# Kernel optimization log

Hardware: AMD Instinct MI355X
Metric: run time of the kernel (lower is better)

Reference implementation:

```python
import jax, jax.numpy as jnp
import numpy as np

NUM_HEADS = 16
HEAD_SIZE = 64
N_EMBD = 1024
BLOCK_SIZE = 2048
B, T = 4, 2048


def setup_inputs() -> dict:
    key = jax.random.key(0)
    ks = jax.random.split(key, 6)
    scale = (N_EMBD * NUM_HEADS) ** (-0.5)
    x = jax.random.normal(ks[0], (B, T, N_EMBD), dtype=jnp.float32)
    Wk = jax.random.normal(ks[1], (NUM_HEADS, N_EMBD, HEAD_SIZE), dtype=jnp.float32) * scale
    Wq = jax.random.normal(ks[2], (NUM_HEADS, N_EMBD, HEAD_SIZE), dtype=jnp.float32) * scale
    Wv = jax.random.normal(ks[3], (NUM_HEADS, N_EMBD, HEAD_SIZE), dtype=jnp.float32) * scale
    proj_w = jax.random.normal(ks[4], (N_EMBD, N_EMBD), dtype=jnp.float32) * (N_EMBD ** -0.5)
    proj_b = jax.random.normal(ks[5], (N_EMBD,), dtype=jnp.float32) * 0.01
    return {"x": x, "Wk": Wk, "Wq": Wq, "Wv": Wv, "proj_w": proj_w, "proj_b": proj_b}


def reference(x, Wk, Wq, Wv, proj_w, proj_b):
    Bsz, Tlen, C = x.shape
    # per-head projections: x [b,t,c] @ W [h,c,d] -> [b,h,t,d]
    q = jnp.einsum('btc,hcd->bhtd', x, Wq)
    k = jnp.einsum('btc,hcd->bhtd', x, Wk)
    v = jnp.einsum('btc,hcd->bhtd', x, Wv)
    wei = jnp.einsum('bhtd,bhsd->bhts', q, k) * (HEAD_SIZE ** -0.5)
    causal = jnp.tril(jnp.ones((Tlen, Tlen), dtype=bool))  # [T,T]
    wei = jnp.where(causal[None, None, :, :], wei, -jnp.inf)
    wei = jax.nn.softmax(wei, axis=-1)
    out = jnp.einsum('bhts,bhsd->bhtd', wei, v)
    out = out.transpose(0, 2, 1, 3).reshape(Bsz, Tlen, NUM_HEADS * HEAD_SIZE)
    out = out @ proj_w.T + proj_b  # nn.Linear: x W^T + b
    return out
```

## Files before the change

kernel.cpp:

```cpp
#include <hip/hip_runtime.h>
#include <hip/hip_bf16.h>

#define BB 4
#define TT 2048
#define CC 1024
#define HH 16
#define DD 64
#define MM (BB * TT)
#define NN_QKV 3072

typedef __attribute__((ext_vector_type(8))) short short8;
typedef __attribute__((ext_vector_type(4))) short short4v;
typedef __attribute__((ext_vector_type(4))) int i32x4;
typedef __attribute__((ext_vector_type(4))) float f32x4;
typedef __attribute__((ext_vector_type(16))) float f32x16;

static __device__ __forceinline__ float exp2_hw(float x) {
  return __builtin_amdgcn_exp2f(x);
}

static __device__ __forceinline__ short f2bf(float f) {
  __hip_bfloat16 h = __float2bfloat16(f);
  short s;
  __builtin_memcpy(&s, &h, 2);
  return s;
}

static __device__ __forceinline__ unsigned int pack2rn(float a, float b) {
  unsigned int ua, ub;
  __builtin_memcpy(&ua, &a, 4);
  __builtin_memcpy(&ub, &b, 4);
  ua += 0x8000u;
  ub += 0x8000u;
  return (ua >> 16) | (ub & 0xFFFF0000u);
}

static __device__ __forceinline__ f32x16 zero16() {
  f32x16 z;
#pragma unroll
  for (int i = 0; i < 16; ++i) z[i] = 0.f;
  return z;
}

static __device__ __forceinline__ int swzv(int d) {
  return (((d & 7) ^ ((d >> 3) & 7)) << 4);
}

static __device__ __forceinline__ void gld16(const void* g, void* l) {
  __builtin_amdgcn_global_load_lds(
      (const __attribute__((address_space(1))) unsigned int*)g,
      (__attribute__((address_space(3))) unsigned int*)l, 16, 0, 0);
}

__global__ __launch_bounds__(256) void cvt8_kernel(const float* __restrict__ in,
                                                   short* __restrict__ out, int n8) {
  int i = blockIdx.x * 256 + threadIdx.x;
  if (i >= n8) return;
  const float4 a = ((const float4*)in)[i * 2];
  const float4 b = ((const float4*)in)[i * 2 + 1];
  short8 o;
  o[0] = f2bf(a.x); o[1] = f2bf(a.y); o[2] = f2bf(a.z); o[3] = f2bf(a.w);
  o[4] = f2bf(b.x); o[5] = f2bf(b.y); o[6] = f2bf(b.z); o[7] = f2bf(b.w);
  ((short8*)out)[i] = o;
}

__global__ __launch_bounds__(256) void cvtw_kernel(
    const float* __restrict__ Wq, const float* __restrict__ Wk,
    const float* __restrict__ Wv, short* __restrict__ Wt) {
  __shared__ float tile[64][65];
  const int tid = threadIdx.x;
  const int h = blockIdx.x;
  const int c0 = blockIdx.y * 64;
  const int sel = blockIdx.z;
  const float* W = (sel == 0) ? Wq : (sel == 1) ? Wk : Wv;

#pragma unroll
  for (int it = 0; it < 16; ++it) {
    int e = it * 256 + tid;
    int cc = e >> 6, d = e & 63;
    tile[d][cc] = W[((size_t)h * CC + c0 + cc) * DD + d];
  }
  __syncthreads();
#pragma unroll
  for (int it = 0; it < 16; ++it) {
    int e = it * 256 + tid;
    int d = e >> 6, cc = e & 63;
    Wt[((size_t)((sel * 16 + h) * 64 + d)) * CC + c0 + cc] = f2bf(tile[d][cc]);
  }
}

template <int MODE>
__global__ __launch_bounds__(256) void gemm32_kernel(
    const short* __restrict__ A, const short* __restrict__ Bt,
    const float* __restrict__ bias,
    __hip_bfloat16* __restrict__ Oq, __hip_bfloat16* __restrict__ Ok,
    __hip_bfloat16* __restrict__ Ov, float* __restrict__ Of) {
  __shared__ __align__(16) char Als[128 * 128];
  __shared__ __align__(16) char Bls[128 * 128];

  const int tid = threadIdx.x;
  const int w = tid >> 6, l = tid & 63;
  const int l31 = l & 31, hi = l >> 5;
  const int wr = w >> 1, wc = w & 1;
  const int m0 = blockIdx.x * 128;
  const int n0 = blockIdx.y * 128;

  const int srow = tid >> 3;
  const int schunk = tid & 7;
  const int sswz = (schunk ^ (srow & 7)) * 8;

  f32x16 acc[2][2];
  acc[0][0] = zero16(); acc[0][1] = zero16();
  acc[1][0] = zero16(); acc[1][1] = zero16();

#pragma unroll 1
  for (int kt = 0; kt < CC; kt += 64) {
    __syncthreads();
#pragma unroll
    for (int i = 0; i < 4; ++i) {
      gld16(A + (size_t)(m0 + i * 32 + srow) * CC + kt + sswz,
            Als + i * 4096 + w * 1024);
      gld16(Bt + (size_t)(n0 + i * 32 + srow) * CC + kt + sswz,
            Bls + i * 4096 + w * 1024);
    }
    __syncthreads();

#pragma unroll
    for (int ks = 0; ks < 4; ++ks) {
      const int c = ks * 2 + hi;
      short8 af[2], bf[2];
#pragma unroll
      for (int mi = 0; mi < 2; ++mi) {
        const int row = wr * 64 + mi * 32 + l31;
        af[mi] = *(const short8*)(Als + row * 128 + ((c ^ (row & 7)) * 16));
      }
#pragma unroll
      for (int ni = 0; ni < 2; ++ni) {
        const int row = wc * 64 + ni * 32 + l31;
        bf[ni] = *(const short8*)(Bls + row * 128 + ((c ^ (row & 7)) * 16));
      }
      __builtin_amdgcn_s_setprio(1);
#pragma unroll
      for (int mi = 0; mi < 2; ++mi)
#pragma unroll
        for (int ni = 0; ni < 2; ++ni)
          acc[mi][ni] = __builtin_amdgcn_mfma_f32_32x32x16_bf16(
              af[mi], bf[ni], acc[mi][ni], 0, 0, 0);
      __builtin_amdgcn_s_setprio(0);
    }
  }

  if (MODE == 0) {
    const int b = m0 >> 11;
#pragma unroll
    for (int ni = 0; ni < 2; ++ni) {
      const int nbase = n0 + wc * 64 + ni * 32;
      const int sel = nbase >> 10;
      const int h = (nbase >> 6) & 15;
      const int d = (nbase & 63) + l31;
      __hip_bfloat16* O = (sel == 0) ? Oq : (sel == 1) ? Ok : Ov;
      const float sc = (sel == 0) ? 0.18033688011112042f : 1.0f;
#pragma unroll
      for (int mi = 0; mi < 2; ++mi) {
#pragma unroll
        for (int r = 0; r < 16; ++r) {
          const int m = m0 + wr * 64 + mi * 32 + (r & 3) + 8 * (r >> 2) + 4 * hi;
          const int t = m & (TT - 1);
          O[(((size_t)b * HH + h) * TT + t) * DD + d] =
              __float2bfloat16(acc[mi][ni][r] * sc);
        }
      }
    }
  } else {
#pragma unroll
    for (int ni = 0; ni < 2; ++ni) {
      const int n = n0 + wc * 64 + ni * 32 + l31;
      const float bv = bias[n];
#pragma unroll
      for (int mi = 0; mi < 2; ++mi) {
#pragma unroll
        for (int r = 0; r < 16; ++r) {
          const int m = m0 + wr * 64 + mi * 32 + (r & 3) + 8 * (r >> 2) + 4 * hi;
          Of[(size_t)m * CC + n] = acc[mi][ni][r] + bv;
        }
      }
    }
  }
}

__global__ __launch_bounds__(512) void attn32_kernel(
    const __hip_bfloat16* __restrict__ qg, const __hip_bfloat16* __restrict__ kg,
    const __hip_bfloat16* __restrict__ vg, __hip_bfloat16* __restrict__ att) {
  __shared__ __align__(16) char LDS[34816];
  char* Ks = LDS;
  char* Vt0 = LDS + 16384;
  char* Vt1 = LDS + 24576;

  const int tid = threadIdx.x;
  const int w = tid >> 6, l = tid & 63;
  const int l31 = l & 31, hi = l >> 5;
  const int w4 = w & 3, g = w >> 2;

  const int flat = blockIdx.x;
  const int r_ = flat >> 6;
  const int qt = (r_ < 4) ? (15 - r_) : (r_ < 8) ? (r_ + 4)
               : (r_ < 12) ? (15 - r_) : (r_ - 12);
  const int hb = flat & 63;
  const int h = hb & 15, b = hb >> 4;
  const size_t base = ((size_t)b * HH + h) * TT * DD;

  const int q0w = qt * 128 + w4 * 32;
  const int myq = q0w + l31;

  const short* Kg = (const short*)kg + base;
  const short* Vg = (const short*)vg + base;
  const int kr = tid >> 3;
  const int kc = tid & 7;
  const int vs = tid >> 3;
  const int vd0 = (tid & 7) * 8;

  const short* Qp = (const short*)qg + base + (size_t)myq * DD;
  const short8 qf0 = *(const short8*)(Qp + 0 + hi * 8);
  const short8 qf1 = *(const short8*)(Qp + 16 + hi * 8);
  const short8 qf2 = *(const short8*)(Qp + 32 + hi * 8);
  const short8 qf3 = *(const short8*)(Qp + 48 + hi * 8);

  f32x16 o0 = zero16(), o1 = zero16();
  float lsum = 0.f;

  const int npair = qt + 1;

#pragma unroll 1
  for (int pt = 0; pt < npair; ++pt) {
    const int sb = pt * 128;

    gld16(Kg + (size_t)(sb + kr) * DD + ((kc ^ (kr & 7)) * 8), Ks + w * 1024);
    gld16(Kg + (size_t)(sb + kr + 64) * DD + ((kc ^ (kr & 7)) * 8),
          Ks + 8192 + w * 1024);
    const short8 va = *(const short8*)(Vg + (size_t)(sb + vs) * DD + vd0);
    const short8 vb = *(const short8*)(Vg + (size_t)(sb + 64 + vs) * DD + vd0);
#pragma unroll
    for (int e = 0; e < 8; ++e) {
      const int d = vd0 + e;
      *(short*)(Vt0 + d * 128 + ((vs * 2) ^ swzv(d))) = va[e];
      *(short*)(Vt1 + d * 128 + ((vs * 2) ^ swzv(d))) = vb[e];
    }
    __syncthreads();

    const int sbg = sb + g * 64;
    const char* Vtg = g ? Vt1 : Vt0;
#pragma unroll
    for (int ks = 0; ks < 2; ++ks) {
      const int sbh = sbg + ks * 32;
      if (sbh > q0w + 31) continue;

      const int krow = g * 64 + ks * 32 + l31;
      const char* Kr = Ks + krow * 128;
      const int rsz = (krow & 7) << 4;
      const short8 kf0 = *(const short8*)(Kr + ((0 * 32 + hi * 16) ^ rsz));
      const short8 kf1 = *(const short8*)(Kr + ((1 * 32 + hi * 16) ^ rsz));
      const short8 kf2 = *(const short8*)(Kr + ((2 * 32 + hi * 16) ^ rsz));
      const short8 kf3 = *(const short8*)(Kr + ((3 * 32 + hi * 16) ^ rsz));
      f32x16 sT = zero16();
      __builtin_amdgcn_s_setprio(1);
      sT = __builtin_amdgcn_mfma_f32_32x32x16_bf16(kf0, qf0, sT, 0, 0, 0);
      sT = __builtin_amdgcn_mfma_f32_32x32x16_bf16(kf1, qf1, sT, 0, 0, 0);
      sT = __builtin_amdgcn_mfma_f32_32x32x16_bf16(kf2, qf2, sT, 0, 0, 0);
      sT = __builtin_amdgcn_mfma_f32_32x32x16_bf16(kf3, qf3, sT, 0, 0, 0);
      __builtin_amdgcn_s_setprio(0);

      float p[16];
      if (sbh == q0w) {
#pragma unroll
        for (int r = 0; r < 16; ++r) {
          const int sg = sbh + (r & 3) + 8 * (r >> 2) + 4 * hi;
          p[r] = (sg > myq) ? -INFINITY : sT[r];
        }
      } else {
#pragma unroll
        for (int r = 0; r < 16; ++r) p[r] = sT[r];
      }

      float ps = 0.f;
#pragma unroll
      for (int r = 0; r < 16; ++r) {
        p[r] = exp2_hw(p[r]);
        ps += p[r];
      }
      lsum += ps;

      unsigned int W[4][2], X[4][2];
#pragma unroll
      for (int qd = 0; qd < 4; ++qd) {
        W[qd][0] = pack2rn(p[4 * qd + 0], p[4 * qd + 1]);
        W[qd][1] = pack2rn(p[4 * qd + 2], p[4 * qd + 3]);
        X[qd][0] = __shfl_xor((int)W[qd][0], 32);
        X[qd][1] = __shfl_xor((int)W[qd][1], 32);
      }

#pragma unroll
      for (int kst = 0; kst < 2; ++kst) {
        union { i32x4 i; short8 s; } A;
        A.i[0] = hi ? (int)X[2 * kst + 1][0] : (int)W[2 * kst][0];
        A.i[1] = hi ? (int)X[2 * kst + 1][1] : (int)W[2 * kst][1];
        A.i[2] = hi ? (int)W[2 * kst + 1][0] : (int)X[2 * kst][0];
        A.i[3] = hi ? (int)W[2 * kst + 1][1] : (int)X[2 * kst][1];
        const int kb = (ks * 32 + kst * 16 + hi * 8) * 2;
        const int r0 = l31, r1 = 32 + l31;
        const short8 vf0 = *(const short8*)(Vtg + r0 * 128 + (kb ^ swzv(r0)));
        const short8 vf1 = *(const short8*)(Vtg + r1 * 128 + (kb ^ swzv(r1)));
        __builtin_amdgcn_s_setprio(1);
        o0 = __builtin_amdgcn_mfma_f32_32x32x16_bf16(vf0, A.s, o0, 0, 0, 0);
        o1 = __builtin_amdgcn_mfma_f32_32x32x16_bf16(vf1, A.s, o1, 0, 0, 0);
        __builtin_amdgcn_s_setprio(0);
      }
    }
    __syncthreads();
  }

  lsum += __shfl_xor(lsum, 32);

  float* comb = (float*)LDS;
  const int idx17 = (w4 * 64 + l) * 17;
  if (g == 1) {
#pragma unroll
    for (int i = 0; i < 16; ++i) comb[idx17 + i] = o0[i];
    comb[idx17 + 16] = lsum;
  }
  __syncthreads();
  if (g == 0) {
#pragma unroll
    for (int i = 0; i < 16; ++i) o0[i] += comb[idx17 + i];
    lsum += comb[idx17 + 16];
  }
  __syncthreads();
  const int idx16 = (w4 * 64 + l) * 16;
  if (g == 1) {
#pragma unroll
    for (int i = 0; i < 16; ++i) comb[idx16 + i] = o1[i];
  }
  __syncthreads();
  if (g == 0) {
#pragma unroll
    for (int i = 0; i < 16; ++i) o1[i] += comb[idx16 + i];

    const float inv = 1.0f / lsum;
    short* orow = (short*)att + ((size_t)b * TT + myq) * CC + h * DD;
#pragma unroll
    for (int j = 0; j < 4; ++j) {
      short4v s0, s1;
#pragma unroll
      for (int i = 0; i < 4; ++i) {
        s0[i] = f2bf(o0[4 * j + i] * inv);
        s1[i] = f2bf(o1[4 * j + i] * inv);
      }
      *(short4v*)(orow + 8 * j + 4 * hi) = s0;
      *(short4v*)(orow + 32 + 8 * j + 4 * hi) = s1;
    }
  }
}

extern "C" void kernel_launch(void* const* d_in, const int* in_sizes, int n_in,
                              void* d_out, int out_size, void* d_ws, size_t ws_size,
                              hipStream_t stream) {
  const float* x  = (const float*)d_in[0];
  const float* Wk = (const float*)d_in[1];
  const float* Wq = (const float*)d_in[2];
  const float* Wv = (const float*)d_in[3];
  const float* pw = (const float*)d_in[4];
  const float* pb = (const float*)d_in[5];
  float* out = (float*)d_out;

  const size_t QE = (size_t)BB * HH * TT * DD;
  __hip_bfloat16* q   = (__hip_bfloat16*)d_ws;
  __hip_bfloat16* k   = q + QE;
  __hip_bfloat16* v   = k + QE;
  short* xbf          = (short*)(v + QE);
  __hip_bfloat16* att = (__hip_bfloat16*)xbf;
  short* Wt           = xbf + QE;
  short* pwbf         = Wt;

  cvt8_kernel<<<(MM * CC / 8 + 255) / 256, 256, 0, stream>>>(x, xbf, MM * CC / 8);
  cvtw_kernel<<<dim3(HH, CC / 64, 3), 256, 0, stream>>>(Wq, Wk, Wv, Wt);
  gemm32_kernel<0><<<dim3(MM / 128, NN_QKV / 128), 256, 0, stream>>>(
      xbf, Wt, nullptr, q, k, v, nullptr);
  attn32_kernel<<<dim3(1024, 1, 1), 512, 0, stream>>>(q, k, v, att);
  cvt8_kernel<<<(CC * CC / 8 + 255) / 256, 256, 0, stream>>>(pw, pwbf, CC * CC / 8);
  gemm32_kernel<1><<<dim3(MM / 128, CC / 128), 256, 0, stream>>>(
      (const short*)att, pwbf, pb, nullptr, nullptr, nullptr, out);
}
```

Baseline: 158.1 us.

## Double-buffer K tiles and prefetch next K/V tile during attention compute

Adds a second LDS buffer for K and issues the global loads for the next 128-key tile (K via direct-to-LDS loads, V into registers) before computing on the current tile. Barriers are replaced with explicit waitcnt plus s_barrier so the prefetch latency overlaps the MFMA work. LDS use grows from about 34 KB to 48 KB per block, which may reduce occupancy, and V is still transposed into a single buffer each iteration.

```diff
diff --git a/kernel.cpp b/kernel.cpp
--- a/kernel.cpp
+++ b/kernel.cpp
@@ -191,10 +191,10 @@
 __global__ __launch_bounds__(512) void attn32_kernel(
     const __hip_bfloat16* __restrict__ qg, const __hip_bfloat16* __restrict__ kg,
     const __hip_bfloat16* __restrict__ vg, __hip_bfloat16* __restrict__ att) {
-  __shared__ __align__(16) char LDS[34816];
+  __shared__ __align__(16) char LDS[49152];
   char* Ks = LDS;
-  char* Vt0 = LDS + 16384;
-  char* Vt1 = LDS + 24576;
+  char* Vt0 = LDS + 32768;
+  char* Vt1 = LDS + 40960;
 
   const int tid = threadIdx.x;
   const int w = tid >> 6, l = tid & 63;
@@ -230,32 +230,50 @@
 
   const int npair = qt + 1;
 
+  gld16(Kg + (size_t)kr * DD + ((kc ^ (kr & 7)) * 8), Ks + w * 1024);
+  gld16(Kg + (size_t)(kr + 64) * DD + ((kc ^ (kr & 7)) * 8),
+        Ks + 8192 + w * 1024);
+  short8 va = *(const short8*)(Vg + (size_t)vs * DD + vd0);
+  short8 vb = *(const short8*)(Vg + (size_t)(64 + vs) * DD + vd0);
+
+  int cur = 0;
 #pragma unroll 1
   for (int pt = 0; pt < npair; ++pt) {
     const int sb = pt * 128;
-
-    gld16(Kg + (size_t)(sb + kr) * DD + ((kc ^ (kr & 7)) * 8), Ks + w * 1024);
-    gld16(Kg + (size_t)(sb + kr + 64) * DD + ((kc ^ (kr & 7)) * 8),
-          Ks + 8192 + w * 1024);
-    const short8 va = *(const short8*)(Vg + (size_t)(sb + vs) * DD + vd0);
-    const short8 vb = *(const short8*)(Vg + (size_t)(sb + 64 + vs) * DD + vd0);
+    const int nxt = cur ^ 1;
+    const bool haveNext = (pt + 1 < npair);
+
+    asm volatile("s_waitcnt vmcnt(0)" ::: "memory");
+
 #pragma unroll
     for (int e = 0; e < 8; ++e) {
       const int d = vd0 + e;
       *(short*)(Vt0 + d * 128 + ((vs * 2) ^ swzv(d))) = va[e];
       *(short*)(Vt1 + d * 128 + ((vs * 2) ^ swzv(d))) = vb[e];
     }
-    __syncthreads();
-
-    const int sbg = sb + g * 64;
+
+    if (haveNext) {
+      const int sb2 = sb + 128;
+      gld16(Kg + (size_t)(sb2 + kr) * DD + ((kc ^ (kr & 7)) * 8),
+            Ks + nxt * 16384 + w * 1024);
+      gld16(Kg + (size_t)(sb2 + kr + 64) * DD + ((kc ^ (kr & 7)) * 8),
+            Ks + nxt * 16384 + 8192 + w * 1024);
+      va = *(const short8*)(Vg + (size_t)(sb2 + vs) * DD + vd0);
+      vb = *(const short8*)(Vg + (size_t)(sb2 + 64 + vs) * DD + vd0);
+    }
+
+    asm volatile("s_waitcnt lgkmcnt(0)" ::: "memory");
+    __builtin_amdgcn_s_barrier();
+
+    const char* Ksb = Ks + cur * 16384;
     const char* Vtg = g ? Vt1 : Vt0;
 #pragma unroll
     for (int ks = 0; ks < 2; ++ks) {
-      const int sbh = sbg + ks * 32;
+      const int sbh = sb + g * 64 + ks * 32;
       if (sbh > q0w + 31) continue;
 
       const int krow = g * 64 + ks * 32 + l31;
-      const char* Kr = Ks + krow * 128;
+      const char* Kr = Ksb + krow * 128;
       const int rsz = (krow & 7) << 4;
       const short8 kf0 = *(const short8*)(Kr + ((0 * 32 + hi * 16) ^ rsz));
       const short8 kf1 = *(const short8*)(Kr + ((1 * 32 + hi * 16) ^ rsz));
@@ -315,7 +333,10 @@
         __builtin_amdgcn_s_setprio(0);
       }
     }
-    __syncthreads();
+
+    asm volatile("" ::: "memory");
+    __builtin_amdgcn_s_barrier();
+    cur = nxt;
   }
 
   lsum += __shfl_xor(lsum, 32);
```

Result: slower. 172.8 us (+9.3%).
